# Performance work log

Hardware: AMD Instinct MI355X
Metric: run time of the kernel (lower is better)

Reference implementation:

```python
import jax, jax.numpy as jnp
import numpy as np

# Model hyperparameters (from __init__)
SIGMA = 0.2
LAMBDA_0 = 1.0
LAMBDA_INF = 0.1
LAMBDA_DECAY = 0.01
MU_J = 0.0
SIGMA_J = 0.3
TOTAL_STEPS = 10000
KAPPA = float(np.exp(MU_J + 0.5 * SIGMA_J ** 2) - 1.0)  # E[e^Y - 1]

# Simulation dims (simulate_path args)
T_TOTAL = 1.0
N_STEPS = 2048
N_PATHS = 32768
DT = T_TOTAL / N_STEPS


def _jump_intensity(t):
    # lambda(t) = lambda_inf + (lambda_0 - lambda_inf) * exp(-decay * t)
    # (t/total_steps * total_steps cancels in the original code)
    return LAMBDA_INF + (LAMBDA_0 - LAMBDA_INF) * jnp.exp(-LAMBDA_DECAY * t)


def setup_inputs() -> dict:
    key = jax.random.key(0)
    k1, k2, k3 = jax.random.split(key, 3)
    # Per-step time-varying Poisson rate for jump counts
    t = jnp.arange(N_STEPS, dtype=jnp.float32) * DT  # (n_steps,)
    lam_dt = _jump_intensity(t) * DT                  # (n_steps,)
    n_jumps = jax.random.poisson(k3, lam_dt[:, None], shape=(N_STEPS, N_PATHS)).astype(jnp.int32)
    return {
        "S0": jnp.ones((1,), dtype=jnp.float32),                         # initial price
        "z_diff": jax.random.normal(k1, (N_STEPS, N_PATHS), jnp.float32),  # Brownian increments / sqrt(dt)
        "z_jump": jax.random.normal(k2, (N_STEPS, N_PATHS), jnp.float32),  # jump-sum normals
        "n_jumps": n_jumps,                                              # Poisson jump counts
    }


def reference(S0, z_diff, z_jump, n_jumps):
    dtype = z_diff.dtype
    t = jnp.arange(N_STEPS, dtype=dtype) * DT          # (n_steps,)
    lam = _jump_intensity(t)[:, None]                   # (n_steps, 1)
    # Sum of n_jumps iid N(mu_J, sigma_J^2) jumps == N(n*mu_J, n*sigma_J^2)
    nj = n_jumps.astype(dtype)
    jump_sizes = nj * MU_J + jnp.sqrt(nj) * SIGMA_J * z_jump
    drift = (0.0 - lam * KAPPA) * DT
    diffusion = SIGMA * jnp.asarray(np.sqrt(DT), dtype) * z_diff
    log_ret = drift + diffusion + jump_sizes            # (n_steps, n_paths)
    log_paths = jnp.cumsum(log_ret, axis=0)             # (n_steps, n_paths)
    log_paths = jnp.concatenate([jnp.zeros((1, log_ret.shape[1]), dtype), log_paths], axis=0)
    paths = (S0[0] * jnp.exp(log_paths)).T              # (n_paths, n_steps + 1)
    return paths
```

## Files before the change

### kernel.cpp

```cpp
#include <hip/hip_runtime.h>
#include <math.h>


#define N_STEPS 2048
#define N_PATHS 32768
#define UROLL 16

#define DT_F 0.00048828125f
#define C_DIFF_F (0.2f * 0.022097086912079608f)
#define KAPPA_F 0.04602785990871629f
#define SIGMA_J_F 0.3f

__device__ __forceinline__ void load_batch(const float* __restrict__ zd_p,
                                           const float* __restrict__ zj_p,
                                           const int* __restrict__ nj_p,
                                           int base, float* zd, float* zj, int* nj) {
#pragma unroll
    for (int i = 0; i < UROLL; ++i) {
        int off = (base + i) * N_PATHS;
        zd[i] = zd_p[off];
        zj[i] = zj_p[off];
        nj[i] = nj_p[off];
    }
}

__device__ __forceinline__ float compute_batch(int base, const float* zd, const float* zj,
                                               const int* nj, float acc, float s0,
                                               float* __restrict__ out_p) {
#pragma unroll
    for (int i = 0; i < UROLL; ++i) {
        int s = base + i;
        float t = (float)s * DT_F;
        float lam = 0.1f + 0.9f * __expf(-0.01f * t);
        float drift = -(lam * KAPPA_F) * DT_F;
        float njf = (float)nj[i];
        float val = (drift + C_DIFF_F * zd[i]) + sqrtf(njf) * SIGMA_J_F * zj[i];
        acc += val;
        out_p[s] = s0 * __expf(acc);
    }
    return acc;
}

__global__ __launch_bounds__(64) void merton_paths_kernel(
    const float* __restrict__ S0,
    const float* __restrict__ z_diff,
    const float* __restrict__ z_jump,
    const int* __restrict__ n_jumps,
    float* __restrict__ out) {
    const int p = blockIdx.x * blockDim.x + threadIdx.x;
    const float s0 = S0[0];

    const float* zd_p = z_diff + p;
    const float* zj_p = z_jump + p;
    const int* nj_p = n_jumps + p;
    float* out_p = out + (long)p * (N_STEPS + 1);

    out_p[0] = s0;
    float* out1 = out_p + 1;

    float zdA[UROLL], zjA[UROLL]; int njA[UROLL];
    float zdB[UROLL], zjB[UROLL]; int njB[UROLL];

    float acc = 0.0f;

    load_batch(zd_p, zj_p, nj_p, 0, zdA, zjA, njA);

    for (int base = 0; base < N_STEPS; base += 2 * UROLL) {
        load_batch(zd_p, zj_p, nj_p, base + UROLL, zdB, zjB, njB);
        acc = compute_batch(base, zdA, zjA, njA, acc, s0, out1);
        if (base + 2 * UROLL < N_STEPS)
            load_batch(zd_p, zj_p, nj_p, base + 2 * UROLL, zdA, zjA, njA);
        acc = compute_batch(base + UROLL, zdB, zjB, njB, acc, s0, out1);
    }
}

extern "C" void kernel_launch(void* const* d_in, const int* in_sizes, int n_in,
                              void* d_out, int out_size, void* d_ws, size_t ws_size,
                              hipStream_t stream) {
    const float* S0      = (const float*)d_in[0];
    const float* z_diff  = (const float*)d_in[1];
    const float* z_jump  = (const float*)d_in[2];
    const int*   n_jumps = (const int*)d_in[3];
    float* out = (float*)d_out;

    dim3 block(64);
    dim3 grid(N_PATHS / 64);
    hipLaunchKernelGGL(merton_paths_kernel, grid, block, 0, stream,
                       S0, z_diff, z_jump, n_jumps, out);
}
```

Measured before the change: 896.7 us.

## Stage output tiles in shared memory for coalesced row-major stores

Each thread used to write its own output row directly, so a wavefront's stores were strided by the row length. The kernel now writes 64-step tiles into a padded shared-memory buffer and then transposes them, so each wavefront stores contiguous chunks of 64 consecutive steps for one path per iteration. It also replaces the per-step exp for the intensity with a running multiplicative recurrence. The trade-offs are two block barriers per tile, shared-memory traffic, and a small accumulated rounding drift in the intensity term.

```diff
diff --git a/kernel.cpp b/kernel.cpp
--- a/kernel.cpp
+++ b/kernel.cpp
@@ -4,19 +4,20 @@
 
 #define N_STEPS 2048
 #define N_PATHS 32768
-#define UROLL 16
+#define U 16
+#define TILE_S 64
+#define ROW (N_STEPS + 1)
 
 #define DT_F 0.00048828125f
-#define C_DIFF_F (0.2f * 0.022097086912079608f)
-#define KAPPA_F 0.04602785990871629f
-#define SIGMA_J_F 0.3f
+#define C_DIFF_F 0.004419417382415922f
+#define KAPPA_F 0.046027859908717f
 
 __device__ __forceinline__ void load_batch(const float* __restrict__ zd_p,
                                            const float* __restrict__ zj_p,
                                            const int* __restrict__ nj_p,
                                            int base, float* zd, float* zj, int* nj) {
 #pragma unroll
-    for (int i = 0; i < UROLL; ++i) {
+    for (int i = 0; i < U; ++i) {
         int off = (base + i) * N_PATHS;
         zd[i] = zd_p[off];
         zj[i] = zj_p[off];
@@ -24,21 +25,20 @@
     }
 }
 
-__device__ __forceinline__ float compute_batch(int base, const float* zd, const float* zj,
-                                               const int* nj, float acc, float s0,
-                                               float* __restrict__ out_p) {
+__device__ __forceinline__ void compute_batch(int jbase, const float* zd, const float* zj,
+                                              const int* nj, float& acc, float& e,
+                                              float r, float s0,
+                                              float* __restrict__ smem_row) {
 #pragma unroll
-    for (int i = 0; i < UROLL; ++i) {
-        int s = base + i;
-        float t = (float)s * DT_F;
-        float lam = 0.1f + 0.9f * __expf(-0.01f * t);
+    for (int i = 0; i < U; ++i) {
+        float lam = 0.1f + 0.9f * e;
+        e *= r;
         float drift = -(lam * KAPPA_F) * DT_F;
         float njf = (float)nj[i];
-        float val = (drift + C_DIFF_F * zd[i]) + sqrtf(njf) * SIGMA_J_F * zj[i];
+        float val = (drift + C_DIFF_F * zd[i]) + sqrtf(njf) * 0.3f * zj[i];
         acc += val;
-        out_p[s] = s0 * __expf(acc);
+        smem_row[jbase + i] = s0 * __expf(acc);
     }
-    return acc;
 }
 
 __global__ __launch_bounds__(64) void merton_paths_kernel(
@@ -47,30 +47,47 @@
     const float* __restrict__ z_jump,
     const int* __restrict__ n_jumps,
     float* __restrict__ out) {
-    const int p = blockIdx.x * blockDim.x + threadIdx.x;
+    const int lane = threadIdx.x;
+    const int pbase = blockIdx.x * 64;
+    const int p = pbase + lane;
     const float s0 = S0[0];
+
+    __shared__ float smem[64][TILE_S + 1];
 
     const float* zd_p = z_diff + p;
     const float* zj_p = z_jump + p;
     const int* nj_p = n_jumps + p;
-    float* out_p = out + (long)p * (N_STEPS + 1);
 
-    out_p[0] = s0;
-    float* out1 = out_p + 1;
+    out[(long)p * ROW] = s0;
 
-    float zdA[UROLL], zjA[UROLL]; int njA[UROLL];
-    float zdB[UROLL], zjB[UROLL]; int njB[UROLL];
+    float zdA[U], zjA[U]; int njA[U];
+    float zdB[U], zjB[U]; int njB[U];
 
     float acc = 0.0f;
+    float e = 1.0f;
+    const float r = __expf(-0.01f * DT_F);
 
     load_batch(zd_p, zj_p, nj_p, 0, zdA, zjA, njA);
 
-    for (int base = 0; base < N_STEPS; base += 2 * UROLL) {
-        load_batch(zd_p, zj_p, nj_p, base + UROLL, zdB, zjB, njB);
-        acc = compute_batch(base, zdA, zjA, njA, acc, s0, out1);
-        if (base + 2 * UROLL < N_STEPS)
-            load_batch(zd_p, zj_p, nj_p, base + 2 * UROLL, zdA, zjA, njA);
-        acc = compute_batch(base + UROLL, zdB, zjB, njB, acc, s0, out1);
+    for (int tb = 0; tb < N_STEPS; tb += TILE_S) {
+        load_batch(zd_p, zj_p, nj_p, tb + U, zdB, zjB, njB);
+        compute_batch(0, zdA, zjA, njA, acc, e, r, s0, smem[lane]);
+        load_batch(zd_p, zj_p, nj_p, tb + 2 * U, zdA, zjA, njA);
+        compute_batch(U, zdB, zjB, njB, acc, e, r, s0, smem[lane]);
+        load_batch(zd_p, zj_p, nj_p, tb + 3 * U, zdB, zjB, njB);
+        compute_batch(2 * U, zdA, zjA, njA, acc, e, r, s0, smem[lane]);
+        if (tb + TILE_S < N_STEPS)
+            load_batch(zd_p, zj_p, nj_p, tb + TILE_S, zdA, zjA, njA);
+        compute_batch(3 * U, zdB, zjB, njB, acc, e, r, s0, smem[lane]);
+
+        __syncthreads();
+        float* orow = out + (long)pbase * ROW + 1 + tb + lane;
+#pragma unroll 16
+        for (int rr = 0; rr < 64; ++rr) {
+            *orow = smem[rr][lane];
+            orow += ROW;
+        }
+        __syncthreads();
     }
 }
 
```

Measured after the change: 877.2 us. -2.2%, faster.
